# Optimization experiments

Hardware: AMD Instinct MI355X
Metric: run time of the kernel (lower is better)

The kernel has to match this reference:

```python
import jax, jax.numpy as jnp
import numpy as np

# Dims: batch=2, seqlen=L=384, d_inner=d=384, d_state=s=384, dt_rank=r=384, d_conv=4.
# NOTE: the original torch module only runs when L == d_inner == d_state == dt_rank
# (see its broadcasting in SelectiveScan and the Linear layer plumbing); we reproduce
# that exact (quirky) broadcast faithfully.
B_, L_, D_, S_, R_, K_ = 2, 384, 384, 384, 384, 4


def setup_inputs() -> dict:
    key = jax.random.key(0)
    ks = jax.random.split(key, 9)
    f32 = jnp.float32
    return {
        "x": jax.random.normal(ks[0], (B_, L_, D_), f32),
        "A_log": jax.random.normal(ks[1], (D_, S_), f32) * 0.02,
        "D": jax.random.normal(ks[2], (D_,), f32) * 0.02,
        "dt_w": jax.random.normal(ks[3], (D_, R_), f32) * 0.02,
        "dt_b": jax.random.normal(ks[4], (D_,), f32) * 0.02,
        "B_w": jax.random.normal(ks[5], (S_, D_), f32) * (1.0 / np.sqrt(D_)),
        "C_w": jax.random.normal(ks[6], (S_, D_), f32) * (1.0 / np.sqrt(D_)),
        "conv_w": jax.random.normal(ks[7], (D_, 1, K_), f32) * (1.0 / np.sqrt(K_)),
        "conv_b": jnp.zeros((D_,), f32),
    }


def _forward(x, A_log, D, dt_w, dt_b, B_w, C_w, conv_w, conv_b):
    b, L, d = x.shape
    A = -jnp.exp(A_log)                       # (d, s)
    dt = jax.nn.softplus(x @ dt_w.T + dt_b)   # (b, L, d)
    x_dbl = x @ B_w.T                         # (b, L, s)
    Bm = x_dbl @ B_w.T                        # (b, L, s)  (module applies B_proj twice)
    Cm = x_dbl @ C_w.T                        # (b, L, s)
    # causal depthwise conv1d: pad (k-1) on the left == torch pad k-1 then [:, :, :L]
    xc = jax.lax.conv_general_dilated(
        x.transpose(0, 2, 1), conv_w, (1,), [(conv_w.shape[-1] - 1, 0)],
        feature_group_count=d, dimension_numbers=("NCH", "OIH", "NCH"))
    xc = xc + conv_b[None, :, None]
    u = jax.nn.silu(xc.transpose(0, 2, 1))    # (b, L, d)
    # selective scan (faithful to the torch SelectiveScan broadcasting)
    deltaA = jnp.exp(dt[..., None] * A[None, None])          # (b, L, d, s)
    deltaB_u = dt[..., None] * Bm[:, None, :, :] * u[..., None]  # (b, L, d, s), needs L==d

    def step(h, inp):
        dA_i, dBu_i, C_i, u_i = inp
        h = dA_i * h + dBu_i                  # (b, d, s)
        y = jnp.sum(h * C_i[:, None, :], -1) + u_i * D  # (b, d)
        return h, y

    h0 = jnp.zeros((b, d, deltaA.shape[-1]), x.dtype)
    xs = (deltaA.transpose(1, 0, 2, 3), deltaB_u.transpose(1, 0, 2, 3),
          Cm.transpose(1, 0, 2), u.transpose(1, 0, 2))
    _, ys = jax.lax.scan(step, h0, xs)        # ys: (L, b, d)
    return ys.transpose(1, 0, 2)


def reference(x, A_log, D, dt_w, dt_b, B_w, C_w, conv_w, conv_b):
    return _forward(x, A_log, D, dt_w, dt_b, B_w, C_w, conv_w, conv_b)
```

## Files before the change

### kernel.cpp

```cpp
#include <hip/hip_runtime.h>
#include <math.h>

#define B_SZ 2
#define L_SZ 384
#define D_SZ 384
#define S_SZ 384
#define BLK_ELEMS (L_SZ * D_SZ)
#define TOT_ELEMS (B_SZ * L_SZ * D_SZ)
#define LOG2E 1.4426950408889634f

typedef __attribute__((ext_vector_type(8))) short bf16x8;
typedef __attribute__((ext_vector_type(4))) float f32x4;
typedef __attribute__((ext_vector_type(2))) float f32x2;

__device__ __forceinline__ float fexp2(float x) {
  return __builtin_amdgcn_exp2f(x);
}
__device__ __forceinline__ float softplus_f(float z) {
  return (z > 20.f) ? z : log1pf(__expf(z));
}
__device__ __forceinline__ unsigned short f2bf(float f) {
  unsigned int u = __float_as_uint(f);
  return (unsigned short)((u + 0x7FFFu + ((u >> 16) & 1u)) >> 16);
}
#define PIPELINE_FENCE() asm volatile("" ::: "memory")

__global__ __launch_bounds__(256) void cvt_bf16_kernel(
    const float* __restrict__ x, const float* __restrict__ dt_w,
    const float* __restrict__ B_w, const float* __restrict__ C_w,
    unsigned short* __restrict__ xbf, unsigned short* __restrict__ dtwbf,
    unsigned short* __restrict__ Bwbf, unsigned short* __restrict__ Cwbf) {
  const int blk = blockIdx.x;
  const float* src;
  unsigned short* dst;
  int base;
  if (blk < 288) { src = x; dst = xbf; base = blk; }
  else if (blk < 432) { src = dt_w; dst = dtwbf; base = blk - 288; }
  else if (blk < 576) { src = B_w; dst = Bwbf; base = blk - 432; }
  else { src = C_w; dst = Cwbf; base = blk - 576; }
  const int idx = base * 1024 + threadIdx.x * 4;
  const float4 v = *(const float4*)(src + idx);
  ushort4 o;
  o.x = f2bf(v.x); o.y = f2bf(v.y); o.z = f2bf(v.z); o.w = f2bf(v.w);
  *(ushort4*)(dst + idx) = o;
}

template <int MODE>
__global__ __launch_bounds__(128, 2) void mfma_dual_gemm(
    const unsigned short* __restrict__ Abf,
    const unsigned short* __restrict__ W1bf,
    const unsigned short* __restrict__ W2bf,
    const float* __restrict__ bias,
    float* __restrict__ O1, void* __restrict__ O2v) {
  __shared__ unsigned short sA[32 * 392];
  __shared__ unsigned short sW1[16 * 392];
  __shared__ unsigned short sW2[16 * 392];

  const int t = threadIdx.x;
  const int wv = t >> 6;
  const int lane = t & 63;
  const int nt = blockIdx.x;
  const int mrow = blockIdx.y;

  const unsigned short* Ab = Abf + mrow * 32 * 384;
  const unsigned short* W1b = W1bf + nt * 16 * 384;
  const unsigned short* W2b = W2bf + nt * 16 * 384;

#pragma unroll
  for (int it = 0; it < 12; ++it) {
    const int id = t + it * 128;
    const int row = id / 48, col = id - row * 48;
    *(bf16x8*)&sA[row * 392 + col * 8] = *(const bf16x8*)(Ab + id * 8);
  }
#pragma unroll
  for (int it = 0; it < 6; ++it) {
    const int id = t + it * 128;
    const int row = id / 48, col = id - row * 48;
    *(bf16x8*)&sW1[row * 392 + col * 8] = *(const bf16x8*)(W1b + id * 8);
    *(bf16x8*)&sW2[row * 392 + col * 8] = *(const bf16x8*)(W2b + id * 8);
  }
  __syncthreads();

  const int rc = lane & 15;
  const int quad = lane >> 4;
  bf16x8 af[12], w1f[12], w2f[12];
#pragma unroll
  for (int kt = 0; kt < 12; ++kt) {
    af[kt] = *(const bf16x8*)&sA[(wv * 16 + rc) * 392 + quad * 8 + kt * 32];
    w1f[kt] = *(const bf16x8*)&sW1[rc * 392 + quad * 8 + kt * 32];
    w2f[kt] = *(const bf16x8*)&sW2[rc * 392 + quad * 8 + kt * 32];
  }
  PIPELINE_FENCE();
  f32x4 acc1 = {0.f, 0.f, 0.f, 0.f};
  f32x4 acc2 = {0.f, 0.f, 0.f, 0.f};
#pragma unroll
  for (int kt = 0; kt < 12; ++kt) {
    acc1 = __builtin_amdgcn_mfma_f32_16x16x32_bf16(af[kt], w1f[kt], acc1, 0, 0, 0);
    acc2 = __builtin_amdgcn_mfma_f32_16x16x32_bf16(af[kt], w2f[kt], acc2, 0, 0, 0);
  }
  const int col = nt * 16 + rc;
  const int row0 = mrow * 32 + wv * 16 + quad * 4;
  if constexpr (MODE == 1) {
    unsigned short* O2 = (unsigned short*)O2v;
    const float bb = bias[col];
#pragma unroll
    for (int r = 0; r < 4; ++r) {
      O1[(row0 + r) * 384 + col] = softplus_f(acc1[r] + bb);
      O2[(row0 + r) * 384 + col] = f2bf(acc2[r]);
    }
  } else {
    float* O2 = (float*)O2v;
#pragma unroll
    for (int r = 0; r < 4; ++r) {
      O1[(row0 + r) * 384 + col] = acc1[r];
      O2[(row0 + r) * 384 + col] = acc2[r];
    }
  }
}

__global__ __launch_bounds__(256) void conv_tr_kernel(
    const float* __restrict__ x, const float* __restrict__ cw,
    const float* __restrict__ cb, const float* __restrict__ dt,
    float* __restrict__ u, float* __restrict__ dt_t,
    float* __restrict__ dtu_t) {
  __shared__ float Tdt[32][33];
  __shared__ float Tdu[32][33];
  const int tx = threadIdx.x;
  const int ty = threadIdx.y;
  const int b = blockIdx.z;
  const int i0 = blockIdx.y * 32;
  const int l0 = blockIdx.x * 32;
  const int gi = i0 + tx;
  const float cbv = cb[gi];
  const float cw0 = cw[gi * 4 + 0], cw1 = cw[gi * 4 + 1];
  const float cw2 = cw[gi * 4 + 2], cw3 = cw[gi * 4 + 3];
#pragma unroll
  for (int r = 0; r < 4; ++r) {
    const int l = l0 + ty + 8 * r;
    float acc = cbv;
    const float x3 = x[(b * L_SZ + l) * D_SZ + gi];
    const float x2 = (l >= 1) ? x[(b * L_SZ + l - 1) * D_SZ + gi] : 0.f;
    const float x1 = (l >= 2) ? x[(b * L_SZ + l - 2) * D_SZ + gi] : 0.f;
    const float x0 = (l >= 3) ? x[(b * L_SZ + l - 3) * D_SZ + gi] : 0.f;
    acc = fmaf(x0, cw0, acc);
    acc = fmaf(x1, cw1, acc);
    acc = fmaf(x2, cw2, acc);
    acc = fmaf(x3, cw3, acc);
    const float uv = acc / (1.f + __expf(-acc));
    const int off = (b * L_SZ + l) * D_SZ + gi;
    u[off] = uv;
    const float dtv = dt[off];
    Tdt[ty + 8 * r][tx] = dtv;
    Tdu[ty + 8 * r][tx] = dtv * uv;
  }
  __syncthreads();
#pragma unroll
  for (int r = 0; r < 4; ++r) {
    const int il = ty + 8 * r;
    const int off = (b * D_SZ + i0 + il) * L_SZ + l0 + tx;
    dt_t[off] = Tdt[tx][il];
    dtu_t[off] = Tdu[tx][il];
  }
}

#define CH 8
struct Chunk {
  f32x4 d0, d1, u0, u1;
  f32x2 c0, c1, c2, c3, c4, c5, c6, c7;
};

#define STR2(x) #x
#define STR(x) STR2(x)

#define LOAD_CHUNK(K, CB, DTB, DUB, IA, IB)                                    \
  {                                                                            \
    asm volatile("global_load_dwordx4 %0, %1, off offset:" STR(IA)             \
                 : "=v"(K.d0) : "v"(DTB));                                     \
    asm volatile("global_load_dwordx4 %0, %1, off offset:" STR(IB)             \
                 : "=v"(K.d1) : "v"(DTB));                                     \
    asm volatile("global_load_dwordx4 %0, %1, off offset:" STR(IA)             \
                 : "=v"(K.u0) : "v"(DUB));                                     \
    asm volatile("global_load_dwordx4 %0, %1, off offset:" STR(IB)             \
                 : "=v"(K.u1) : "v"(DUB));                                     \
    const float* b1_ = (CB) + 1152;                                            \
    const float* b2_ = (CB) + 2304;                                            \
    asm volatile("global_load_dwordx2 %0, %1, off" : "=v"(K.c0) : "v"(CB));    \
    asm volatile("global_load_dwordx2 %0, %1, off offset:1536"                 \
                 : "=v"(K.c1) : "v"(CB));                                      \
    asm volatile("global_load_dwordx2 %0, %1, off offset:3072"                 \
                 : "=v"(K.c2) : "v"(CB));                                      \
    asm volatile("global_load_dwordx2 %0, %1, off" : "=v"(K.c3) : "v"(b1_));   \
    asm volatile("global_load_dwordx2 %0, %1, off offset:1536"                 \
                 : "=v"(K.c4) : "v"(b1_));                                     \
    asm volatile("global_load_dwordx2 %0, %1, off offset:3072"                 \
                 : "=v"(K.c5) : "v"(b1_));                                     \
    asm volatile("global_load_dwordx2 %0, %1, off" : "=v"(K.c6) : "v"(b2_));   \
    asm volatile("global_load_dwordx2 %0, %1, off offset:1536"                 \
                 : "=v"(K.c7) : "v"(b2_));                                     \
  }

#define WAIT_CHUNK(K)                                                          \
  asm volatile("s_waitcnt vmcnt(24)"                                           \
               : "+v"(K.d0), "+v"(K.d1), "+v"(K.u0), "+v"(K.u1), "+v"(K.c0),   \
                 "+v"(K.c1), "+v"(K.c2), "+v"(K.c3), "+v"(K.c4), "+v"(K.c5),   \
                 "+v"(K.c6), "+v"(K.c7))

__global__ __launch_bounds__(256, 3) void scan_kernel(
    const float* __restrict__ A_log, const float* __restrict__ dt_t,
    const float* __restrict__ dtu_t, const float* __restrict__ Bm,
    const float* __restrict__ Cm, float* __restrict__ part) {
  const int wid = ((blockIdx.x << 8) + (int)threadIdx.x) >> 6;
  const int lane = threadIdx.x & 63;
  const int w = wid % 3;
  const int sid = wid / 3;
  const int b = sid / D_SZ;
  const int i = sid % D_SZ;
  const int j0 = w * 128 + 2 * lane;

  const float2 av = *(const float2*)(A_log + i * S_SZ + j0);
  const float2 bv = *(const float2*)(Bm + (b * D_SZ + i) * S_SZ + j0);
  float a20 = -__expf(av.x) * LOG2E;
  float a21 = -__expf(av.y) * LOG2E;
  float bw0 = bv.x, bw1 = bv.y;
  float h0 = 0.f, h1 = 0.f;

  const float* dtR = dt_t + (b * D_SZ + i) * L_SZ;
  const float* duR = dtu_t + (b * D_SZ + i) * L_SZ;
  const float* cC = Cm + b * BLK_ELEMS + j0;
  float* pp = part + ((w * B_SZ + b) * D_SZ + i) * L_SZ;

  const int sidx = ((lane & 1) << 2) | (lane & 2) | ((lane >> 2) & 1);
  const bool storer = lane < 8;

  asm volatile("" :: "v"(a20), "v"(a21), "v"(bw0), "v"(bw1));
  asm volatile("s_waitcnt vmcnt(0)");

  float accs[8];
#define SSTEP(s, DT, DU, CC)                          \
  {                                                   \
    const float e0 = fexp2((DT)*a20);                 \
    const float e1 = fexp2((DT)*a21);                 \
    h0 = fmaf(e0, h0, bw0 * (DU));                    \
    h1 = fmaf(e1, h1, bw1 * (DU));                    \
    accs[s] = fmaf(h1, (CC)[1], h0 * (CC)[0]);        \
  }

  auto compute_chunk = [&](const Chunk& K, int l0) {
    SSTEP(0, K.d0[0], K.u0[0], K.c0);
    SSTEP(1, K.d0[1], K.u0[1], K.c1);
    SSTEP(2, K.d0[2], K.u0[2], K.c2);
    SSTEP(3, K.d0[3], K.u0[3], K.c3);
    SSTEP(4, K.d1[0], K.u1[0], K.c4);
    SSTEP(5, K.d1[1], K.u1[1], K.c5);
    SSTEP(6, K.d1[2], K.u1[2], K.c6);
    SSTEP(7, K.d1[3], K.u1[3], K.c7);
    {
      const bool s1 = (lane & 1) != 0;
#pragma unroll
      for (int q = 0; q < 4; ++q) {
        const float keep = s1 ? accs[q + 4] : accs[q];
        const float send = s1 ? accs[q] : accs[q + 4];
        accs[q] = keep + __shfl_xor(send, 1, 64);
      }
      const bool s2 = (lane & 2) != 0;
#pragma unroll
      for (int q = 0; q < 2; ++q) {
        const float keep = s2 ? accs[q + 2] : accs[q];
        const float send = s2 ? accs[q] : accs[q + 2];
        accs[q] = keep + __shfl_xor(send, 2, 64);
      }
      const bool s3 = (lane & 4) != 0;
      {
        const float keep = s3 ? accs[1] : accs[0];
        const float send = s3 ? accs[0] : accs[1];
        accs[0] = keep + __shfl_xor(send, 4, 64);
      }
    }
    float r = accs[0];
    r += __shfl_xor(r, 8, 64);
    r += __shfl_xor(r, 16, 64);
    r += __shfl_xor(r, 32, 64);
    if (storer) pp[l0 + sidx] = r;
  };

  Chunk K0, K1, K2;
  LOAD_CHUNK(K0, cC, dtR, duR, 0, 16);
  cC += 3072;
  LOAD_CHUNK(K1, cC, dtR, duR, 32, 48);
  cC += 3072;
  for (int it = 0; it < 16; ++it) {
    const int l0 = it * 24;
    LOAD_CHUNK(K2, cC, dtR, duR, 64, 80);
    cC += 3072;
    WAIT_CHUNK(K0);
    compute_chunk(K0, l0);
    LOAD_CHUNK(K0, cC, dtR, duR, 96, 112);
    cC += 3072;
    WAIT_CHUNK(K1);
    compute_chunk(K1, l0 + 8);
    LOAD_CHUNK(K1, cC, dtR, duR, 128, 144);
    cC += 3072;
    WAIT_CHUNK(K2);
    compute_chunk(K2, l0 + 16);
    dtR += 24;
    duR += 24;
  }
#undef SSTEP
}

__global__ __launch_bounds__(256) void combine_kernel(
    const float* __restrict__ part, const float* __restrict__ u,
    const float* __restrict__ Dv, float* __restrict__ y) {
  __shared__ float T[32][33];
  const int tx = threadIdx.x;
  const int ty0 = threadIdx.y;
  const int b = blockIdx.z;
  const int i0 = blockIdx.y * 32;
  const int l0 = blockIdx.x * 32;
#pragma unroll
  for (int r = 0; r < 4; ++r) {
    const int il = ty0 + 8 * r;
    float s = 0.f;
#pragma unroll
    for (int w = 0; w < 3; ++w)
      s += part[((w * B_SZ + b) * D_SZ + i0 + il) * L_SZ + l0 + tx];
    T[il][tx] = s;
  }
  __syncthreads();
#pragma unroll
  for (int r = 0; r < 4; ++r) {
    const int ll = ty0 + 8 * r;
    const int gi = i0 + tx;
    const int off = (b * L_SZ + l0 + ll) * D_SZ + gi;
    y[off] = fmaf(u[off], Dv[gi], T[tx][ll]);
  }
}

extern "C" void kernel_launch(void* const* d_in, const int* in_sizes, int n_in,
                              void* d_out, int out_size, void* d_ws,
                              size_t ws_size, hipStream_t stream) {
  const float* x = (const float*)d_in[0];
  const float* A_log = (const float*)d_in[1];
  const float* D = (const float*)d_in[2];
  const float* dt_w = (const float*)d_in[3];
  const float* dt_b = (const float*)d_in[4];
  const float* B_w = (const float*)d_in[5];
  const float* C_w = (const float*)d_in[6];
  const float* conv_w = (const float*)d_in[7];
  const float* conv_b = (const float*)d_in[8];
  float* y = (float*)d_out;

  float* ws = (float*)d_ws;
  float* dt = ws;
  float* u = ws + TOT_ELEMS;
  float* Bm = ws + 2 * TOT_ELEMS;
  float* Cm = ws + 3 * TOT_ELEMS;
  float* dt_t = ws + 4 * TOT_ELEMS;
  float* dtu_t = ws + 5 * TOT_ELEMS;
  float* part = ws + 6 * TOT_ELEMS;
  unsigned short* bfarea = (unsigned short*)(ws + 10 * TOT_ELEMS);
  unsigned short* xbf = bfarea;
  unsigned short* dtwbf = bfarea + 294912;
  unsigned short* Bwbf = bfarea + 442368;
  unsigned short* Cwbf = bfarea + 589824;
  unsigned short* xdblbf = bfarea + 737280;

  cvt_bf16_kernel<<<720, 256, 0, stream>>>(x, dt_w, B_w, C_w, xbf, dtwbf, Bwbf, Cwbf);
  mfma_dual_gemm<1><<<dim3(24, 24), 128, 0, stream>>>(xbf, dtwbf, Bwbf, dt_b, dt, xdblbf);
  mfma_dual_gemm<2><<<dim3(24, 24), 128, 0, stream>>>(xdblbf, Bwbf, Cwbf, nullptr, Bm, Cm);
  conv_tr_kernel<<<dim3(L_SZ / 32, D_SZ / 32, B_SZ), dim3(32, 8), 0, stream>>>(
      x, conv_w, conv_b, dt, u, dt_t, dtu_t);
  scan_kernel<<<576, 256, 0, stream>>>(A_log, dt_t, dtu_t, Bm, Cm, part);
  combine_kernel<<<dim3(L_SZ / 32, D_SZ / 32, B_SZ), dim3(32, 8), 0, stream>>>(
      part, u, D, y);
}
```

Measured before the change: 148.8 us.

## Restructure scan so each wave handles two channels with shared C loads

Each wave now handles two d-channels across 64 state columns, one state per lane, instead of one channel across 128 states with two per lane. The C values loaded per step are reused for both channels, and dt/dtu come in as one coalesced dword per lane that is broadcast with readlane. Chunks grow to 16 timesteps, the cross-lane reduction becomes a 32-value transpose-reduce, and the state is split six ways with the combine kernel summing six partials. This roughly halves C-matrix traffic per channel, at the cost of more partial-sum writes, more shuffles, higher register pressure and a larger workspace.

```diff
diff --git a/kernel.cpp b/kernel.cpp
--- a/kernel.cpp
+++ b/kernel.cpp
@@ -11,7 +11,6 @@
 
 typedef __attribute__((ext_vector_type(8))) short bf16x8;
 typedef __attribute__((ext_vector_type(4))) float f32x4;
-typedef __attribute__((ext_vector_type(2))) float f32x2;
 
 __device__ __forceinline__ float fexp2(float x) {
   return __builtin_amdgcn_exp2f(x);
@@ -163,149 +162,158 @@
   }
 }
 
-#define CH 8
-struct Chunk {
-  f32x4 d0, d1, u0, u1;
-  f32x2 c0, c1, c2, c3, c4, c5, c6, c7;
+struct ChunkV {
+  float combo;
+  float c[16];
 };
 
-#define STR2(x) #x
-#define STR(x) STR2(x)
-
-#define LOAD_CHUNK(K, CB, DTB, DUB, IA, IB)                                    \
+#define LOAD_CHUNK(K, B0, B1, B2, B3, B4, B5, CMB)                             \
   {                                                                            \
-    asm volatile("global_load_dwordx4 %0, %1, off offset:" STR(IA)             \
-                 : "=v"(K.d0) : "v"(DTB));                                     \
-    asm volatile("global_load_dwordx4 %0, %1, off offset:" STR(IB)             \
-                 : "=v"(K.d1) : "v"(DTB));                                     \
-    asm volatile("global_load_dwordx4 %0, %1, off offset:" STR(IA)             \
-                 : "=v"(K.u0) : "v"(DUB));                                     \
-    asm volatile("global_load_dwordx4 %0, %1, off offset:" STR(IB)             \
-                 : "=v"(K.u1) : "v"(DUB));                                     \
-    const float* b1_ = (CB) + 1152;                                            \
-    const float* b2_ = (CB) + 2304;                                            \
-    asm volatile("global_load_dwordx2 %0, %1, off" : "=v"(K.c0) : "v"(CB));    \
-    asm volatile("global_load_dwordx2 %0, %1, off offset:1536"                 \
-                 : "=v"(K.c1) : "v"(CB));                                      \
-    asm volatile("global_load_dwordx2 %0, %1, off offset:3072"                 \
-                 : "=v"(K.c2) : "v"(CB));                                      \
-    asm volatile("global_load_dwordx2 %0, %1, off" : "=v"(K.c3) : "v"(b1_));   \
-    asm volatile("global_load_dwordx2 %0, %1, off offset:1536"                 \
-                 : "=v"(K.c4) : "v"(b1_));                                     \
-    asm volatile("global_load_dwordx2 %0, %1, off offset:3072"                 \
-                 : "=v"(K.c5) : "v"(b1_));                                     \
-    asm volatile("global_load_dwordx2 %0, %1, off" : "=v"(K.c6) : "v"(b2_));   \
-    asm volatile("global_load_dwordx2 %0, %1, off offset:1536"                 \
-                 : "=v"(K.c7) : "v"(b2_));                                     \
+    asm volatile("global_load_dword %0, %1, off" : "=v"(K.combo) : "v"(CMB));  \
+    asm volatile("global_load_dword %0, %1, off" : "=v"(K.c[0]) : "v"(B0));    \
+    asm volatile("global_load_dword %0, %1, off offset:1536"                   \
+                 : "=v"(K.c[1]) : "v"(B0));                                    \
+    asm volatile("global_load_dword %0, %1, off offset:3072"                   \
+                 : "=v"(K.c[2]) : "v"(B0));                                    \
+    asm volatile("global_load_dword %0, %1, off" : "=v"(K.c[3]) : "v"(B1));    \
+    asm volatile("global_load_dword %0, %1, off offset:1536"                   \
+                 : "=v"(K.c[4]) : "v"(B1));                                    \
+    asm volatile("global_load_dword %0, %1, off offset:3072"                   \
+                 : "=v"(K.c[5]) : "v"(B1));                                    \
+    asm volatile("global_load_dword %0, %1, off" : "=v"(K.c[6]) : "v"(B2));    \
+    asm volatile("global_load_dword %0, %1, off offset:1536"                   \
+                 : "=v"(K.c[7]) : "v"(B2));                                    \
+    asm volatile("global_load_dword %0, %1, off offset:3072"                   \
+                 : "=v"(K.c[8]) : "v"(B2));                                    \
+    asm volatile("global_load_dword %0, %1, off" : "=v"(K.c[9]) : "v"(B3));    \
+    asm volatile("global_load_dword %0, %1, off offset:1536"                   \
+                 : "=v"(K.c[10]) : "v"(B3));                                   \
+    asm volatile("global_load_dword %0, %1, off offset:3072"                   \
+                 : "=v"(K.c[11]) : "v"(B3));                                   \
+    asm volatile("global_load_dword %0, %1, off" : "=v"(K.c[12]) : "v"(B4));   \
+    asm volatile("global_load_dword %0, %1, off offset:1536"                   \
+                 : "=v"(K.c[13]) : "v"(B4));                                   \
+    asm volatile("global_load_dword %0, %1, off offset:3072"                   \
+                 : "=v"(K.c[14]) : "v"(B4));                                   \
+    asm volatile("global_load_dword %0, %1, off" : "=v"(K.c[15]) : "v"(B5));   \
   }
 
 #define WAIT_CHUNK(K)                                                          \
-  asm volatile("s_waitcnt vmcnt(24)"                                           \
-               : "+v"(K.d0), "+v"(K.d1), "+v"(K.u0), "+v"(K.u1), "+v"(K.c0),   \
-                 "+v"(K.c1), "+v"(K.c2), "+v"(K.c3), "+v"(K.c4), "+v"(K.c5),   \
-                 "+v"(K.c6), "+v"(K.c7))
-
-__global__ __launch_bounds__(256, 3) void scan_kernel(
+  asm volatile("s_waitcnt vmcnt(34)"                                           \
+               : "+v"(K.combo), "+v"(K.c[0]), "+v"(K.c[1]), "+v"(K.c[2]),      \
+                 "+v"(K.c[3]), "+v"(K.c[4]), "+v"(K.c[5]), "+v"(K.c[6]),       \
+                 "+v"(K.c[7]), "+v"(K.c[8]), "+v"(K.c[9]), "+v"(K.c[10]),      \
+                 "+v"(K.c[11]), "+v"(K.c[12]), "+v"(K.c[13]), "+v"(K.c[14]),   \
+                 "+v"(K.c[15]))
+
+#define ADV_BASES()                                                            \
+  {                                                                            \
+    cb0 += 6144; cb1 += 6144; cb2 += 6144;                                     \
+    cb3 += 6144; cb4 += 6144; cb5 += 6144; cmb += 16;                          \
+  }
+
+__global__ __launch_bounds__(192, 3) void scan_kernel(
     const float* __restrict__ A_log, const float* __restrict__ dt_t,
     const float* __restrict__ dtu_t, const float* __restrict__ Bm,
     const float* __restrict__ Cm, float* __restrict__ part) {
-  const int wid = ((blockIdx.x << 8) + (int)threadIdx.x) >> 6;
+  const int wave = blockIdx.x * 3 + (threadIdx.x >> 6);
   const int lane = threadIdx.x & 63;
-  const int w = wid % 3;
-  const int sid = wid / 3;
-  const int b = sid / D_SZ;
-  const int i = sid % D_SZ;
-  const int j0 = w * 128 + 2 * lane;
-
-  const float2 av = *(const float2*)(A_log + i * S_SZ + j0);
-  const float2 bv = *(const float2*)(Bm + (b * D_SZ + i) * S_SZ + j0);
-  float a20 = -__expf(av.x) * LOG2E;
-  float a21 = -__expf(av.y) * LOG2E;
-  float bw0 = bv.x, bw1 = bv.y;
+  const int w = wave % 6;
+  const int grp = wave / 6;
+  const int b = grp / 192;
+  const int i0 = (grp % 192) * 2;
+  const int j = w * 64 + lane;
+
+  const float al0 = A_log[(i0 + 0) * S_SZ + j];
+  const float al1 = A_log[(i0 + 1) * S_SZ + j];
+  const float bw0 = Bm[(b * D_SZ + i0 + 0) * S_SZ + j];
+  const float bw1 = Bm[(b * D_SZ + i0 + 1) * S_SZ + j];
+  const float a20 = -__expf(al0) * LOG2E;
+  const float a21 = -__expf(al1) * LOG2E;
   float h0 = 0.f, h1 = 0.f;
 
-  const float* dtR = dt_t + (b * D_SZ + i) * L_SZ;
-  const float* duR = dtu_t + (b * D_SZ + i) * L_SZ;
-  const float* cC = Cm + b * BLK_ELEMS + j0;
-  float* pp = part + ((w * B_SZ + b) * D_SZ + i) * L_SZ;
-
-  const int sidx = ((lane & 1) << 2) | (lane & 2) | ((lane >> 2) & 1);
-  const bool storer = lane < 8;
+  const int var = lane >> 5;
+  const int cch = (lane >> 4) & 1;
+  const int cs = lane & 15;
+  const float* cmb =
+      (var ? dtu_t : dt_t) + (b * D_SZ + i0 + cch) * L_SZ + cs;
+
+  const float* cmrow = Cm + b * BLK_ELEMS + j;
+  const float* cb0 = cmrow;
+  const float* cb1 = cmrow + 3 * D_SZ;
+  const float* cb2 = cmrow + 6 * D_SZ;
+  const float* cb3 = cmrow + 9 * D_SZ;
+  const float* cb4 = cmrow + 12 * D_SZ;
+  const float* cb5 = cmrow + 15 * D_SZ;
+
+  const int k = ((lane & 1) << 4) | ((lane & 2) << 2) | (lane & 4) |
+                ((lane & 8) >> 2) | ((lane & 16) >> 4);
+  float* pstore =
+      part + ((w * B_SZ + b) * D_SZ + i0) * L_SZ + (k >> 4) * L_SZ + (k & 15);
+  const bool storer = lane < 32;
 
   asm volatile("" :: "v"(a20), "v"(a21), "v"(bw0), "v"(bw1));
   asm volatile("s_waitcnt vmcnt(0)");
 
-  float accs[8];
-#define SSTEP(s, DT, DU, CC)                          \
-  {                                                   \
-    const float e0 = fexp2((DT)*a20);                 \
-    const float e1 = fexp2((DT)*a21);                 \
-    h0 = fmaf(e0, h0, bw0 * (DU));                    \
-    h1 = fmaf(e1, h1, bw1 * (DU));                    \
-    accs[s] = fmaf(h1, (CC)[1], h0 * (CC)[0]);        \
-  }
-
-  auto compute_chunk = [&](const Chunk& K, int l0) {
-    SSTEP(0, K.d0[0], K.u0[0], K.c0);
-    SSTEP(1, K.d0[1], K.u0[1], K.c1);
-    SSTEP(2, K.d0[2], K.u0[2], K.c2);
-    SSTEP(3, K.d0[3], K.u0[3], K.c3);
-    SSTEP(4, K.d1[0], K.u1[0], K.c4);
-    SSTEP(5, K.d1[1], K.u1[1], K.c5);
-    SSTEP(6, K.d1[2], K.u1[2], K.c6);
-    SSTEP(7, K.d1[3], K.u1[3], K.c7);
-    {
-      const bool s1 = (lane & 1) != 0;
-#pragma unroll
-      for (int q = 0; q < 4; ++q) {
-        const float keep = s1 ? accs[q + 4] : accs[q];
-        const float send = s1 ? accs[q] : accs[q + 4];
-        accs[q] = keep + __shfl_xor(send, 1, 64);
-      }
-      const bool s2 = (lane & 2) != 0;
-#pragma unroll
-      for (int q = 0; q < 2; ++q) {
-        const float keep = s2 ? accs[q + 2] : accs[q];
-        const float send = s2 ? accs[q] : accs[q + 2];
-        accs[q] = keep + __shfl_xor(send, 2, 64);
-      }
-      const bool s3 = (lane & 4) != 0;
-      {
-        const float keep = s3 ? accs[1] : accs[0];
-        const float send = s3 ? accs[0] : accs[1];
-        accs[0] = keep + __shfl_xor(send, 4, 64);
+  auto compute_chunk = [&](ChunkV& K) {
+    float acc[32];
+    const int combo_i = __float_as_int(K.combo);
+#pragma unroll
+    for (int s = 0; s < 16; ++s) {
+      const float dt0 = __int_as_float(__builtin_amdgcn_readlane(combo_i, s));
+      const float dt1 =
+          __int_as_float(__builtin_amdgcn_readlane(combo_i, 16 + s));
+      const float du0 =
+          __int_as_float(__builtin_amdgcn_readlane(combo_i, 32 + s));
+      const float du1 =
+          __int_as_float(__builtin_amdgcn_readlane(combo_i, 48 + s));
+      const float e0 = fexp2(dt0 * a20);
+      const float e1 = fexp2(dt1 * a21);
+      h0 = fmaf(e0, h0, bw0 * du0);
+      h1 = fmaf(e1, h1, bw1 * du1);
+      acc[s] = h0 * K.c[s];
+      acc[16 + s] = h1 * K.c[s];
+    }
+#pragma unroll
+    for (int st = 0; st < 5; ++st) {
+      const int d = 1 << st;
+      const int n2 = 16 >> st;
+      const bool hi = (lane & d) != 0;
+#pragma unroll
+      for (int q = 0; q < 16; ++q) {
+        if (q < n2) {
+          const float keep = hi ? acc[q + n2] : acc[q];
+          const float send = hi ? acc[q] : acc[q + n2];
+          acc[q] = keep + __shfl_xor(send, d, 64);
+        }
       }
     }
-    float r = accs[0];
-    r += __shfl_xor(r, 8, 64);
-    r += __shfl_xor(r, 16, 64);
+    float r = acc[0];
     r += __shfl_xor(r, 32, 64);
-    if (storer) pp[l0 + sidx] = r;
+    if (storer) *pstore = r;
+    pstore += 16;
   };
 
-  Chunk K0, K1, K2;
-  LOAD_CHUNK(K0, cC, dtR, duR, 0, 16);
-  cC += 3072;
-  LOAD_CHUNK(K1, cC, dtR, duR, 32, 48);
-  cC += 3072;
-  for (int it = 0; it < 16; ++it) {
-    const int l0 = it * 24;
-    LOAD_CHUNK(K2, cC, dtR, duR, 64, 80);
-    cC += 3072;
+  ChunkV K0, K1, K2;
+  LOAD_CHUNK(K0, cb0, cb1, cb2, cb3, cb4, cb5, cmb);
+  ADV_BASES();
+  LOAD_CHUNK(K1, cb0, cb1, cb2, cb3, cb4, cb5, cmb);
+  ADV_BASES();
+#pragma unroll 1
+  for (int mit = 0; mit < 8; ++mit) {
+    LOAD_CHUNK(K2, cb0, cb1, cb2, cb3, cb4, cb5, cmb);
+    ADV_BASES();
     WAIT_CHUNK(K0);
-    compute_chunk(K0, l0);
-    LOAD_CHUNK(K0, cC, dtR, duR, 96, 112);
-    cC += 3072;
+    compute_chunk(K0);
+    LOAD_CHUNK(K0, cb0, cb1, cb2, cb3, cb4, cb5, cmb);
+    ADV_BASES();
     WAIT_CHUNK(K1);
-    compute_chunk(K1, l0 + 8);
-    LOAD_CHUNK(K1, cC, dtR, duR, 128, 144);
-    cC += 3072;
+    compute_chunk(K1);
+    LOAD_CHUNK(K1, cb0, cb1, cb2, cb3, cb4, cb5, cmb);
+    ADV_BASES();
     WAIT_CHUNK(K2);
-    compute_chunk(K2, l0 + 16);
-    dtR += 24;
-    duR += 24;
-  }
-#undef SSTEP
+    compute_chunk(K2);
+  }
 }
 
 __global__ __launch_bounds__(256) void combine_kernel(
@@ -322,7 +330,7 @@
     const int il = ty0 + 8 * r;
     float s = 0.f;
 #pragma unroll
-    for (int w = 0; w < 3; ++w)
+    for (int w = 0; w < 6; ++w)
       s += part[((w * B_SZ + b) * D_SZ + i0 + il) * L_SZ + l0 + tx];
     T[il][tx] = s;
   }
@@ -358,7 +366,7 @@
   float* dt_t = ws + 4 * TOT_ELEMS;
   float* dtu_t = ws + 5 * TOT_ELEMS;
   float* part = ws + 6 * TOT_ELEMS;
-  unsigned short* bfarea = (unsigned short*)(ws + 10 * TOT_ELEMS);
+  unsigned short* bfarea = (unsigned short*)(ws + 12 * TOT_ELEMS);
   unsigned short* xbf = bfarea;
   unsigned short* dtwbf = bfarea + 294912;
   unsigned short* Bwbf = bfarea + 442368;
@@ -370,7 +378,7 @@
   mfma_dual_gemm<2><<<dim3(24, 24), 128, 0, stream>>>(xdblbf, Bwbf, Cwbf, nullptr, Bm, Cm);
   conv_tr_kernel<<<dim3(L_SZ / 32, D_SZ / 32, B_SZ), dim3(32, 8), 0, stream>>>(
       x, conv_w, conv_b, dt, u, dt_t, dtu_t);
-  scan_kernel<<<576, 256, 0, stream>>>(A_log, dt_t, dtu_t, Bm, Cm, part);
+  scan_kernel<<<768, 192, 0, stream>>>(A_log, dt_t, dtu_t, Bm, Cm, part);
   combine_kernel<<<dim3(L_SZ / 32, D_SZ / 32, B_SZ), dim3(32, 8), 0, stream>>>(
       part, u, D, y);
 }
```

New measurement: 143.4 us. 3.6% less time.
